# Kernel tuning notes

Hardware: AMD Instinct MI355X
Metric: run time of the kernel (lower is better)

Reference implementation:

```python
import jax, jax.numpy as jnp
import numpy as np

D_MODEL = 256
NUM_HEADS = 4
N = 2048           # num points (N == M required by the rotary theta sharing)
K_LIST = [0.5]     # per-layer top-k fraction (module's self.k)


def setup_inputs() -> dict:
    key = jax.random.key(0)
    ks = jax.random.split(key, 10)
    s = 0.05
    return {
        "input_q": jax.random.normal(ks[0], (1, N, D_MODEL), jnp.float32),
        "input_k": jax.random.normal(ks[1], (1, N, D_MODEL), jnp.float32),
        "input_v": jax.random.normal(ks[2], (1, N, D_MODEL), jnp.float32),
        "embed_qk": jax.random.normal(ks[3], (1, N, D_MODEL // 2), jnp.float32),
        "Wq": jax.random.normal(ks[4], (D_MODEL, D_MODEL), jnp.float32) * s,
        "bq": jnp.zeros((D_MODEL,), jnp.float32),
        "Wk": jax.random.normal(ks[5], (D_MODEL, D_MODEL), jnp.float32) * s,
        "bk": jnp.zeros((D_MODEL,), jnp.float32),
        "Wv": jax.random.normal(ks[6], (D_MODEL, D_MODEL), jnp.float32) * s,
        "bv": jnp.zeros((D_MODEL,), jnp.float32),
        "layer": 0,
    }


def _rotary(x, theta_half):
    # x: (b,h,n,d); theta_half: (b,h,n,d//2)
    b, h, n, d = x.shape
    xr = x.reshape(b, h, n, d // 2, 2)
    rot = jnp.stack([-xr[..., 1], xr[..., 0]], axis=-1).reshape(b, h, n, d)
    # F.interpolate(scale_factor=2, mode='nearest') == repeat each element twice
    theta = jnp.repeat(theta_half, 2, axis=-1)
    return x * jnp.cos(theta) + rot * jnp.sin(theta)


def reference(input_q, input_k, input_v, embed_qk, Wq, bq, Wk, bk, Wv, bv, layer):
    b, n, dm = input_q.shape
    h = NUM_HEADS
    dh = dm // h

    def split_heads(x):  # (b,n,dm) -> (b,h,n,dh)
        return x.reshape(b, -1, h, dh).transpose(0, 2, 1, 3)

    q = split_heads(input_q @ Wq.T + bq)
    k = split_heads(input_k @ Wk.T + bk)
    v = split_heads(input_v @ Wv.T + bv)
    theta_half = embed_qk.reshape(b, -1, h, dh // 2).transpose(0, 2, 1, 3)
    q = _rotary(q, theta_half)
    k = _rotary(k, theta_half)

    scores = jnp.einsum('bhnd,bhmd->bhnm', q, k) / jnp.sqrt(jnp.float32(dh))
    kk = int(n * K_LIST[layer])  # top-k size
    vals, idx = jax.lax.top_k(scores, kk)          # (b,h,n,kk)
    prob = jax.nn.softmax(vals, axis=-1)
    bI = jnp.arange(b)[:, None, None, None]
    hI = jnp.arange(h)[None, :, None, None]
    nI = jnp.arange(n)[None, None, :, None]
    sparse = jnp.zeros_like(scores).at[bI, hI, nI, idx].set(prob)
    hidden = jnp.einsum('bhnm,bhmd->bhnd', sparse, v)
    hidden = hidden.transpose(0, 2, 1, 3).reshape(b, n, dm)
    return hidden, sparse
```

## Files before the change

kernel.cpp:

```cpp
#include <hip/hip_runtime.h>
#include <hip/hip_bf16.h>
#include <stdint.h>

#define NPTS 2048
#define DM 256
#define NH 4
#define DH 64
#define KK 1024

#define QH_OFF 0
#define QL_OFF (NH*NPTS*DH)
#define KH_OFF (2*NH*NPTS*DH)
#define KL_OFF (3*NH*NPTS*DH)
#define VT_OFF (4*NH*NPTS*DH)

typedef __attribute__((ext_vector_type(8)))  short bf16x8;
typedef __attribute__((ext_vector_type(4)))  float f32x4;
typedef __attribute__((ext_vector_type(16))) float f32x16;

__device__ inline ushort bf16rn(float f) {
    uint32_t u = __float_as_uint(f);
    uint32_t r = (u + 0x7FFFu + ((u >> 16) & 1u)) >> 16;
    return (ushort)r;
}
__device__ inline float bf16tof(ushort h) {
    return __uint_as_float(((uint32_t)h) << 16);
}

__global__ __launch_bounds__(256) void proj_rope_kernel(
    const float* __restrict__ xq, const float* __restrict__ xk, const float* __restrict__ xv,
    const float* __restrict__ emb,
    const float* __restrict__ Wq, const float* __restrict__ bq,
    const float* __restrict__ Wk, const float* __restrict__ bk,
    const float* __restrict__ Wv, const float* __restrict__ bv,
    ushort* __restrict__ wsu)
{
    const int z = blockIdx.y;
    const int n0 = blockIdx.x * 8;
    const float* X = (z==0) ? xq : (z==1) ? xk : xv;
    const float* W = (z==0) ? Wq : (z==1) ? Wk : Wv;
    const float* B = (z==0) ? bq : (z==1) ? bk : bv;

    __shared__ float s_in[8][DM];
    {
        const float4* X4 = (const float4*)(X + (size_t)n0 * DM);
        float4* s4 = (float4*)&s_in[0][0];
        #pragma unroll
        for (int i = 0; i < 2; i++) {
            int f = threadIdx.x + 256*i;
            s4[f] = X4[f];
        }
    }
    __syncthreads();

    const int c = threadIdx.x;
    const int h = c >> 6, d = c & 63;
    const float bias = B[c];
    float acc[8];
    #pragma unroll
    for (int r = 0; r < 8; r++) acc[r] = bias;

    const float4* W4 = (const float4*)(W + (size_t)c * DM);
    #pragma unroll 4
    for (int k4 = 0; k4 < DM/4; k4++) {
        float4 w = W4[k4];
        #pragma unroll
        for (int r = 0; r < 8; r++) {
            float4 sv = *(const float4*)&s_in[r][k4*4];
            acc[r] = fmaf(sv.x, w.x, acc[r]);
            acc[r] = fmaf(sv.y, w.y, acc[r]);
            acc[r] = fmaf(sv.z, w.z, acc[r]);
            acc[r] = fmaf(sv.w, w.w, acc[r]);
        }
    }

    if (z < 2) {
        const int p = d >> 1;
        #pragma unroll
        for (int r = 0; r < 8; r++) {
            float th = emb[(size_t)(n0 + r)*(DM/2) + h*32 + p];
            float cs = cosf(th), sn = sinf(th);
            float partner = __shfl_xor(acc[r], 1);
            acc[r] = (d & 1) ? (acc[r]*cs + partner*sn) : (acc[r]*cs - partner*sn);
            if (z == 0) acc[r] *= 0.125f;
        }
        ushort* hi = wsu + ((z==0) ? QH_OFF : KH_OFF);
        ushort* lo = wsu + ((z==0) ? QL_OFF : KL_OFF);
        #pragma unroll
        for (int r = 0; r < 8; r++) {
            size_t idx = ((size_t)(h*NPTS + n0 + r))*DH + d;
            ushort hb = bf16rn(acc[r]);
            float res = acc[r] - bf16tof(hb);
            hi[idx] = hb;
            lo[idx] = bf16rn(res);
        }
    } else {
        __syncthreads();
        #pragma unroll
        for (int r = 0; r < 8; r++) s_in[r][c] = acc[r];
        __syncthreads();
        ushort tmp[8];
        #pragma unroll
        for (int r = 0; r < 8; r++) tmp[r] = bf16rn(s_in[r][c]);
        *(bf16x8*)(wsu + VT_OFF + (size_t)c*NPTS + n0) = *(bf16x8*)tmp;
    }
}

__global__ __launch_bounds__(256) void scores_mfma_kernel(const ushort* __restrict__ wsu, float* __restrict__ sp)
{
    const ushort* qh = wsu + QH_OFF;
    const ushort* ql = wsu + QL_OFF;
    const ushort* kh = wsu + KH_OFF;
    const ushort* kl = wsu + KL_OFF;

    const int h = blockIdx.z;
    const int rbase = blockIdx.y * 64;
    const int cbase = blockIdx.x * 256;
    const int w = threadIdx.x >> 6, l = threadIdx.x & 63;
    const int r0 = rbase + (w & 1)*32;
    const int c0 = cbase + (w >> 1)*128;
    const int lr = l & 31, g = l >> 5;

    const size_t abase = ((size_t)(h*NPTS + r0 + lr))*DH + 8*g;
    bf16x8 a_h[4], a_l[4];
    #pragma unroll
    for (int s = 0; s < 4; s++) {
        a_h[s] = *(const bf16x8*)(qh + abase + 16*s);
        a_l[s] = *(const bf16x8*)(ql + abase + 16*s);
    }

    f32x16 acc[4];
    #pragma unroll
    for (int t = 0; t < 4; t++)
        #pragma unroll
        for (int e = 0; e < 16; e++) acc[t][e] = 0.f;

    #pragma unroll
    for (int t = 0; t < 4; t++) {
        const size_t bbase = ((size_t)(h*NPTS + c0 + t*32 + lr))*DH + 8*g;
        #pragma unroll
        for (int s = 0; s < 4; s++) {
            bf16x8 bh = *(const bf16x8*)(kh + bbase + 16*s);
            bf16x8 bl = *(const bf16x8*)(kl + bbase + 16*s);
            acc[t] = __builtin_amdgcn_mfma_f32_32x32x16_bf16(a_h[s], bh, acc[t], 0, 0, 0);
            acc[t] = __builtin_amdgcn_mfma_f32_32x32x16_bf16(a_h[s], bl, acc[t], 0, 0, 0);
            acc[t] = __builtin_amdgcn_mfma_f32_32x32x16_bf16(a_l[s], bh, acc[t], 0, 0, 0);
        }
    }

    #pragma unroll
    for (int t = 0; t < 4; t++) {
        const int col = c0 + t*32 + lr;
        #pragma unroll
        for (int reg = 0; reg < 16; reg++) {
            const int row = r0 + 4*g + (reg & 3) + 8*(reg >> 2);
            sp[((size_t)(h*NPTS + row))*NPTS + col] = acc[t][reg];
        }
    }
}

__device__ inline uint32_t f2u(float f) {
    uint32_t x = __float_as_uint(f);
    return (x & 0x80000000u) ? ~x : (x | 0x80000000u);
}
__device__ inline float u2f(uint32_t u) {
    uint32_t x = (u & 0x80000000u) ? (u ^ 0x80000000u) : ~u;
    return __uint_as_float(x);
}

__global__ __launch_bounds__(512, 6) void topk_attend_kernel(const ushort* __restrict__ wsu, float* __restrict__ out)
{
    const int h  = blockIdx.y;
    const int n0 = blockIdx.x * 8;
    float* sp = out + (size_t)NPTS*DM;
    __shared__ ushort s_p[8][NPTS];
    __shared__ float s_hid[8][8][DH];

    const int wave = threadIdx.x >> 6, lane = threadIdx.x & 63;
    const int row = wave;

    float* grow = sp + ((size_t)(h*NPTS + n0 + row))*NPTS;
    uint32_t u[32];
    #pragma unroll
    for (int j = 0; j < 8; j++) {
        float4 v = ((const float4*)grow)[lane + 64*j];
        u[4*j+0] = f2u(v.x); u[4*j+1] = f2u(v.y); u[4*j+2] = f2u(v.z); u[4*j+3] = f2u(v.w);
    }

    uint32_t mu = 0u;
    #pragma unroll
    for (int j = 0; j < 32; j++) mu = (u[j] > mu) ? u[j] : mu;
    #pragma unroll
    for (int off = 32; off; off >>= 1) {
        uint32_t o = (uint32_t)__shfl_xor((int)mu, off);
        mu = (o > mu) ? o : mu;
    }
    const float mx = u2f(mu);

    uint32_t cur = 0u;
    for (int bit = 31; bit >= 0; bit--) {
        uint32_t cand = cur | (1u << bit);
        int c = 0;
        #pragma unroll
        for (int j = 0; j < 32; j++) c += (int)__popcll(__ballot(u[j] >= cand));
        if (c >= KK) { cur = cand; if (c == KK) break; }
    }

    float zsum = 0.f;
    #pragma unroll
    for (int j = 0; j < 32; j++) {
        bool sel = (u[j] >= cur);
        float f = u2f(u[j]);
        float ev = sel ? __expf(f - mx) : 0.f;
        u[j] = __float_as_uint(ev);
        zsum += ev;
    }
    #pragma unroll
    for (int off = 32; off; off >>= 1) zsum += __shfl_xor(zsum, off);
    const float rz = 1.f / zsum;

    char* srow = (char*)&s_p[row][0];
    const uint32_t swz = (uint32_t)((row & 7) << 4);
    #pragma unroll
    for (int j = 0; j < 8; j++) {
        float4 p;
        p.x = __uint_as_float(u[4*j+0]) * rz;
        p.y = __uint_as_float(u[4*j+1]) * rz;
        p.z = __uint_as_float(u[4*j+2]) * rz;
        p.w = __uint_as_float(u[4*j+3]) * rz;
        ((float4*)grow)[lane + 64*j] = p;
        uint32_t pk0 = ((uint32_t)bf16rn(p.y) << 16) | bf16rn(p.x);
        uint32_t pk1 = ((uint32_t)bf16rn(p.w) << 16) | bf16rn(p.z);
        uint32_t boff = (8u*lane + 512u*j) ^ swz;
        *(uint2*)(srow + boff) = make_uint2(pk0, pk1);
    }
    __syncthreads();

    const ushort* Vt = wsu + VT_OFF + (size_t)h*DH*NPTS;
    const int m0 = wave * 256;
    const int cg = lane >> 4;
    const int cl = lane & 15;
    const int prow = cl & 7;
    f32x4 pacc[4];
    #pragma unroll
    for (int dt = 0; dt < 4; dt++) pacc[dt] = (f32x4){0.f,0.f,0.f,0.f};

    const char* pbase = (const char*)&s_p[prow][0];
    const uint32_t pswz = (uint32_t)((prow & 7) << 4);
    for (int s = 0; s < 8; s++) {
        const int mk = m0 + 32*s + 8*cg;
        uint32_t boff = ((uint32_t)(2*mk)) ^ pswz;
        bf16x8 bfrag = *(const bf16x8*)(pbase + boff);
        #pragma unroll
        for (int dt = 0; dt < 4; dt++) {
            bf16x8 afrag = *(const bf16x8*)(Vt + ((size_t)(16*dt + cl))*NPTS + mk);
            pacc[dt] = __builtin_amdgcn_mfma_f32_16x16x32_bf16(afrag, bfrag, pacc[dt], 0, 0, 0);
        }
    }
    if (cl < 8) {
        #pragma unroll
        for (int dt = 0; dt < 4; dt++)
            #pragma unroll
            for (int reg = 0; reg < 4; reg++)
                s_hid[wave][cl][16*dt + 4*cg + reg] = pacc[dt][reg];
    }
    __syncthreads();

    {
        int idx = threadIdx.x;
        int r = idx >> 6, dd = idx & 63;
        float s = 0.f;
        #pragma unroll
        for (int c2 = 0; c2 < 8; c2++) s += s_hid[c2][r][dd];
        out[(size_t)(n0 + r)*DM + h*DH + dd] = s;
    }
}

extern "C" void kernel_launch(void* const* d_in, const int* in_sizes, int n_in,
                              void* d_out, int out_size, void* d_ws, size_t ws_size,
                              hipStream_t stream)
{
    const float* xq  = (const float*)d_in[0];
    const float* xk  = (const float*)d_in[1];
    const float* xv  = (const float*)d_in[2];
    const float* emb = (const float*)d_in[3];
    const float* Wq  = (const float*)d_in[4];
    const float* bq  = (const float*)d_in[5];
    const float* Wk  = (const float*)d_in[6];
    const float* bk  = (const float*)d_in[7];
    const float* Wv  = (const float*)d_in[8];
    const float* bv  = (const float*)d_in[9];
    float* out  = (float*)d_out;
    ushort* wsu = (ushort*)d_ws;

    proj_rope_kernel<<<dim3(NPTS/8, 3), 256, 0, stream>>>(xq, xk, xv, emb, Wq, bq, Wk, bk, Wv, bv, wsu);
    scores_mfma_kernel<<<dim3(NPTS/256, NPTS/64, NH), 256, 0, stream>>>(wsu, out + (size_t)NPTS*DM);
    topk_attend_kernel<<<dim3(NPTS/8, NH), 512, 0, stream>>>(wsu, out);
}
```

Before: 115.9 us.

## Fuse QK scores into top-k attention kernel via shared-memory score tile

Merges the separate scores kernel into the top-k/attend kernel. Each block computes its 8 score rows with 16x16 MFMAs straight into a swizzled 64KB LDS buffer, so the full fp32 score matrix no longer makes a round trip through global memory. The same buffer is then reused for the bf16 probabilities and the partial hidden sums. The radix select now resolves two bits per pass, with three ballot counts per pass, and the first V fragment is prefetched before the barrier. The cost is a 64KB LDS footprint with a lower occupancy hint, and each block re-reads all K rows for its head.

```diff
diff --git a/kernel.cpp b/kernel.cpp
--- a/kernel.cpp
+++ b/kernel.cpp
@@ -16,7 +16,6 @@
 
 typedef __attribute__((ext_vector_type(8)))  short bf16x8;
 typedef __attribute__((ext_vector_type(4)))  float f32x4;
-typedef __attribute__((ext_vector_type(16))) float f32x16;
 
 __device__ inline ushort bf16rn(float f) {
     uint32_t u = __float_as_uint(f);
@@ -25,6 +24,14 @@
 }
 __device__ inline float bf16tof(ushort h) {
     return __uint_as_float(((uint32_t)h) << 16);
+}
+__device__ inline uint32_t f2u(float f) {
+    uint32_t x = __float_as_uint(f);
+    return (x & 0x80000000u) ? ~x : (x | 0x80000000u);
+}
+__device__ inline float u2f(uint32_t u) {
+    uint32_t x = (u & 0x80000000u) ? (u ^ 0x80000000u) : ~u;
+    return __uint_as_float(x);
 }
 
 __global__ __launch_bounds__(256) void proj_rope_kernel(
@@ -106,85 +113,61 @@
     }
 }
 
-__global__ __launch_bounds__(256) void scores_mfma_kernel(const ushort* __restrict__ wsu, float* __restrict__ sp)
-{
-    const ushort* qh = wsu + QH_OFF;
-    const ushort* ql = wsu + QL_OFF;
-    const ushort* kh = wsu + KH_OFF;
-    const ushort* kl = wsu + KL_OFF;
-
-    const int h = blockIdx.z;
-    const int rbase = blockIdx.y * 64;
-    const int cbase = blockIdx.x * 256;
-    const int w = threadIdx.x >> 6, l = threadIdx.x & 63;
-    const int r0 = rbase + (w & 1)*32;
-    const int c0 = cbase + (w >> 1)*128;
-    const int lr = l & 31, g = l >> 5;
-
-    const size_t abase = ((size_t)(h*NPTS + r0 + lr))*DH + 8*g;
-    bf16x8 a_h[4], a_l[4];
-    #pragma unroll
-    for (int s = 0; s < 4; s++) {
-        a_h[s] = *(const bf16x8*)(qh + abase + 16*s);
-        a_l[s] = *(const bf16x8*)(ql + abase + 16*s);
-    }
-
-    f32x16 acc[4];
-    #pragma unroll
-    for (int t = 0; t < 4; t++)
-        #pragma unroll
-        for (int e = 0; e < 16; e++) acc[t][e] = 0.f;
-
-    #pragma unroll
-    for (int t = 0; t < 4; t++) {
-        const size_t bbase = ((size_t)(h*NPTS + c0 + t*32 + lr))*DH + 8*g;
-        #pragma unroll
-        for (int s = 0; s < 4; s++) {
-            bf16x8 bh = *(const bf16x8*)(kh + bbase + 16*s);
-            bf16x8 bl = *(const bf16x8*)(kl + bbase + 16*s);
-            acc[t] = __builtin_amdgcn_mfma_f32_32x32x16_bf16(a_h[s], bh, acc[t], 0, 0, 0);
-            acc[t] = __builtin_amdgcn_mfma_f32_32x32x16_bf16(a_h[s], bl, acc[t], 0, 0, 0);
-            acc[t] = __builtin_amdgcn_mfma_f32_32x32x16_bf16(a_l[s], bh, acc[t], 0, 0, 0);
-        }
-    }
-
-    #pragma unroll
-    for (int t = 0; t < 4; t++) {
-        const int col = c0 + t*32 + lr;
-        #pragma unroll
-        for (int reg = 0; reg < 16; reg++) {
-            const int row = r0 + 4*g + (reg & 3) + 8*(reg >> 2);
-            sp[((size_t)(h*NPTS + row))*NPTS + col] = acc[t][reg];
-        }
-    }
-}
-
-__device__ inline uint32_t f2u(float f) {
-    uint32_t x = __float_as_uint(f);
-    return (x & 0x80000000u) ? ~x : (x | 0x80000000u);
-}
-__device__ inline float u2f(uint32_t u) {
-    uint32_t x = (u & 0x80000000u) ? (u ^ 0x80000000u) : ~u;
-    return __uint_as_float(x);
-}
-
-__global__ __launch_bounds__(512, 6) void topk_attend_kernel(const ushort* __restrict__ wsu, float* __restrict__ out)
+__global__ __launch_bounds__(512, 4) void fused_attn_kernel(const ushort* __restrict__ wsu,
+                                                            float* __restrict__ out)
 {
     const int h  = blockIdx.y;
     const int n0 = blockIdx.x * 8;
     float* sp = out + (size_t)NPTS*DM;
-    __shared__ ushort s_p[8][NPTS];
-    __shared__ float s_hid[8][8][DH];
-
-    const int wave = threadIdx.x >> 6, lane = threadIdx.x & 63;
-    const int row = wave;
-
-    float* grow = sp + ((size_t)(h*NPTS + n0 + row))*NPTS;
+    __shared__ float S[8][NPTS];
+
+    const int w  = threadIdx.x >> 6, l = threadIdx.x & 63;
+    const int cl = l & 15, cg = l >> 4;
+
+    {
+        const size_t qbase = ((size_t)(h*NPTS + n0 + (cl & 7)))*DH + 8*cg;
+        bf16x8 qbh[2], qbl[2];
+        #pragma unroll
+        for (int s = 0; s < 2; s++) {
+            qbh[s] = *(const bf16x8*)(wsu + QH_OFF + qbase + 32*s);
+            qbl[s] = *(const bf16x8*)(wsu + QL_OFF + qbase + 32*s);
+        }
+        const int col0 = 256*w;
+        #pragma unroll 4
+        for (int t = 0; t < 16; t++) {
+            const size_t kbase = ((size_t)(h*NPTS + col0 + 16*t + cl))*DH + 8*cg;
+            f32x4 acc = {0.f, 0.f, 0.f, 0.f};
+            #pragma unroll
+            for (int s = 0; s < 2; s++) {
+                bf16x8 ah = *(const bf16x8*)(wsu + KH_OFF + kbase + 32*s);
+                bf16x8 al = *(const bf16x8*)(wsu + KL_OFF + kbase + 32*s);
+                acc = __builtin_amdgcn_mfma_f32_16x16x32_bf16(ah, qbh[s], acc, 0, 0, 0);
+                acc = __builtin_amdgcn_mfma_f32_16x16x32_bf16(ah, qbl[s], acc, 0, 0, 0);
+                acc = __builtin_amdgcn_mfma_f32_16x16x32_bf16(al, qbh[s], acc, 0, 0, 0);
+            }
+            if (cl < 8) {
+                uint32_t byte = (1024u*(uint32_t)w + 64u*(uint32_t)t + 16u*(uint32_t)cg)
+                                ^ ((uint32_t)cl << 4);
+                *(f32x4*)((char*)&S[cl][0] + byte) = acc;
+            }
+        }
+    }
+
+    const ushort* Vt = wsu + VT_OFF + (size_t)h*DH*NPTS;
+    const int m0 = w * 256;
+    bf16x8 vpre[4];
+    #pragma unroll
+    for (int dt = 0; dt < 4; dt++)
+        vpre[dt] = *(const bf16x8*)(Vt + ((size_t)(16*dt + cl))*NPTS + (m0 + 8*cg));
+
+    __syncthreads();
+
+    const uint32_t sw = ((uint32_t)w) << 4;
     uint32_t u[32];
     #pragma unroll
     for (int j = 0; j < 8; j++) {
-        float4 v = ((const float4*)grow)[lane + 64*j];
-        u[4*j+0] = f2u(v.x); u[4*j+1] = f2u(v.y); u[4*j+2] = f2u(v.z); u[4*j+3] = f2u(v.w);
+        f32x4 v = *(const f32x4*)((const char*)&S[w][0] + ((16u*(uint32_t)(l + 64*j)) ^ sw));
+        u[4*j+0] = f2u(v[0]); u[4*j+1] = f2u(v[1]); u[4*j+2] = f2u(v[2]); u[4*j+3] = f2u(v[3]);
     }
 
     uint32_t mu = 0u;
@@ -198,20 +181,27 @@
     const float mx = u2f(mu);
 
     uint32_t cur = 0u;
-    for (int bit = 31; bit >= 0; bit--) {
-        uint32_t cand = cur | (1u << bit);
-        int c = 0;
-        #pragma unroll
-        for (int j = 0; j < 32; j++) c += (int)__popcll(__ballot(u[j] >= cand));
-        if (c >= KK) { cur = cand; if (c == KK) break; }
+    for (int bit = 30; bit >= 0; bit -= 2) {
+        const uint32_t cA = cur | (3u << bit);
+        const uint32_t cB = cur | (2u << bit);
+        const uint32_t cC = cur | (1u << bit);
+        int nA = 0, nB = 0, nC = 0;
+        #pragma unroll
+        for (int j = 0; j < 32; j++) {
+            nA += (int)__popcll(__ballot(u[j] >= cA));
+            nB += (int)__popcll(__ballot(u[j] >= cB));
+            nC += (int)__popcll(__ballot(u[j] >= cC));
+        }
+        if (nA >= KK)      { cur = cA; if (nA == KK) break; }
+        else if (nB >= KK) { cur = cB; if (nB == KK) break; }
+        else if (nC >= KK) { cur = cC; if (nC == KK) break; }
     }
 
     float zsum = 0.f;
     #pragma unroll
     for (int j = 0; j < 32; j++) {
         bool sel = (u[j] >= cur);
-        float f = u2f(u[j]);
-        float ev = sel ? __expf(f - mx) : 0.f;
+        float ev = sel ? __expf(u2f(u[j]) - mx) : 0.f;
         u[j] = __float_as_uint(ev);
         zsum += ev;
     }
@@ -219,8 +209,7 @@
     for (int off = 32; off; off >>= 1) zsum += __shfl_xor(zsum, off);
     const float rz = 1.f / zsum;
 
-    char* srow = (char*)&s_p[row][0];
-    const uint32_t swz = (uint32_t)((row & 7) << 4);
+    float* grow = sp + ((size_t)(h*NPTS + n0 + w))*NPTS;
     #pragma unroll
     for (int j = 0; j < 8; j++) {
         float4 p;
@@ -228,51 +217,53 @@
         p.y = __uint_as_float(u[4*j+1]) * rz;
         p.z = __uint_as_float(u[4*j+2]) * rz;
         p.w = __uint_as_float(u[4*j+3]) * rz;
-        ((float4*)grow)[lane + 64*j] = p;
-        uint32_t pk0 = ((uint32_t)bf16rn(p.y) << 16) | bf16rn(p.x);
-        uint32_t pk1 = ((uint32_t)bf16rn(p.w) << 16) | bf16rn(p.z);
-        uint32_t boff = (8u*lane + 512u*j) ^ swz;
-        *(uint2*)(srow + boff) = make_uint2(pk0, pk1);
-    }
-    __syncthreads();
-
-    const ushort* Vt = wsu + VT_OFF + (size_t)h*DH*NPTS;
-    const int m0 = wave * 256;
-    const int cg = lane >> 4;
-    const int cl = lane & 15;
+        ((float4*)grow)[l + 64*j] = p;
+        uint32_t pk0 = ((uint32_t)bf16rn(p.y) << 16) | (uint32_t)bf16rn(p.x);
+        uint32_t pk1 = ((uint32_t)bf16rn(p.w) << 16) | (uint32_t)bf16rn(p.z);
+        *(uint2*)((char*)&S[w][0] + ((8u*(uint32_t)(l + 64*j)) ^ sw)) = make_uint2(pk0, pk1);
+    }
+    __syncthreads();
+
     const int prow = cl & 7;
+    const char* pbase = (const char*)&S[prow][0];
+    const uint32_t psw = ((uint32_t)prow) << 4;
     f32x4 pacc[4];
     #pragma unroll
-    for (int dt = 0; dt < 4; dt++) pacc[dt] = (f32x4){0.f,0.f,0.f,0.f};
-
-    const char* pbase = (const char*)&s_p[prow][0];
-    const uint32_t pswz = (uint32_t)((prow & 7) << 4);
-    for (int s = 0; s < 8; s++) {
+    for (int dt = 0; dt < 4; dt++) pacc[dt] = (f32x4){0.f, 0.f, 0.f, 0.f};
+
+    {
+        bf16x8 bfrag = *(const bf16x8*)(pbase + ((2u*(uint32_t)(m0 + 8*cg)) ^ psw));
+        #pragma unroll
+        for (int dt = 0; dt < 4; dt++)
+            pacc[dt] = __builtin_amdgcn_mfma_f32_16x16x32_bf16(vpre[dt], bfrag, pacc[dt], 0, 0, 0);
+    }
+    for (int s = 1; s < 8; s++) {
         const int mk = m0 + 32*s + 8*cg;
-        uint32_t boff = ((uint32_t)(2*mk)) ^ pswz;
-        bf16x8 bfrag = *(const bf16x8*)(pbase + boff);
+        bf16x8 bfrag = *(const bf16x8*)(pbase + ((2u*(uint32_t)mk) ^ psw));
         #pragma unroll
         for (int dt = 0; dt < 4; dt++) {
             bf16x8 afrag = *(const bf16x8*)(Vt + ((size_t)(16*dt + cl))*NPTS + mk);
             pacc[dt] = __builtin_amdgcn_mfma_f32_16x16x32_bf16(afrag, bfrag, pacc[dt], 0, 0, 0);
         }
     }
+
     if (cl < 8) {
+        float* part = (float*)((char*)S + (size_t)w*(NPTS*4) + 4096);
         #pragma unroll
         for (int dt = 0; dt < 4; dt++)
             #pragma unroll
-            for (int reg = 0; reg < 4; reg++)
-                s_hid[wave][cl][16*dt + 4*cg + reg] = pacc[dt][reg];
-    }
-    __syncthreads();
-
-    {
-        int idx = threadIdx.x;
-        int r = idx >> 6, dd = idx & 63;
-        float s = 0.f;
-        #pragma unroll
-        for (int c2 = 0; c2 < 8; c2++) s += s_hid[c2][r][dd];
-        out[(size_t)(n0 + r)*DM + h*DH + dd] = s;
+            for (int r4 = 0; r4 < 4; r4++)
+                part[cl*68 + 16*dt + 4*cg + r4] = pacc[dt][r4];
+    }
+    __syncthreads();
+
+    {
+        const int r = w, d = l;
+        float ssum = 0.f;
+        #pragma unroll
+        for (int wv = 0; wv < 8; wv++)
+            ssum += *(const float*)((const char*)S + (size_t)wv*(NPTS*4) + 4096 + 4u*(uint32_t)(r*68 + d));
+        out[(size_t)(n0 + r)*DM + h*DH + d] = ssum;
     }
 }
 
@@ -294,6 +285,5 @@
     ushort* wsu = (ushort*)d_ws;
 
     proj_rope_kernel<<<dim3(NPTS/8, 3), 256, 0, stream>>>(xq, xk, xv, emb, Wq, bq, Wk, bk, Wv, bv, wsu);
-    scores_mfma_kernel<<<dim3(NPTS/256, NPTS/64, NH), 256, 0, stream>>>(wsu, out + (size_t)NPTS*DM);
-    topk_attend_kernel<<<dim3(NPTS/8, NH), 512, 0, stream>>>(wsu, out);
-}
+    fused_attn_kernel<<<dim3(NPTS/8, NH), 512, 0, stream>>>(wsu, out);
+}
```

Result: slower. 143.2 us (+23.6%).
